# Kernel tuning notes

Measured on AMD Instinct MI355X. Metric: run time of the kernel, lower is better.

Reference implementation:

```python
import jax, jax.numpy as jnp
import numpy as np

NUM_PROMPTS = 20
PROMPT_DIM = 1024
BATCH = 32768
EPS = 1e-12  # F.normalize eps


def _l2_normalize(x):
    # matches torch F.normalize: x / max(||x||, eps)
    n = jnp.linalg.norm(x, axis=-1, keepdims=True)
    return x / jnp.maximum(n, EPS)


def setup_inputs() -> dict:
    key = jax.random.key(0)
    k1, k2, k3 = jax.random.split(key, 3)
    input_data = jax.random.normal(k1, (BATCH, PROMPT_DIM), dtype=jnp.float32)
    prompt_keys = jax.random.normal(k2, (NUM_PROMPTS, PROMPT_DIM), dtype=jnp.float32) * 0.01
    prompt_values = jax.random.normal(k3, (NUM_PROMPTS, PROMPT_DIM), dtype=jnp.float32)
    return {"input_data": input_data, "prompt_keys": prompt_keys,
            "prompt_values": prompt_values, "top_k": 5}


def reference(input_data, prompt_keys, prompt_values, top_k):
    # residual_strategy with use_prompt_threshhold=False: all samples stay
    # active for exactly top_k steps.
    norm_keys = _l2_normalize(prompt_keys)  # [P, D]
    residual = input_data                   # [B, D]
    selected, indices = [], []
    commitment = jnp.zeros((input_data.shape[0],), dtype=input_data.dtype)
    for _ in range(top_k):  # small fixed loop (top_k=5)
        sims = _l2_normalize(residual) @ norm_keys.T          # [B, P] cosine sim
        probs = jax.nn.softmax(sims, axis=1)                  # [B, P]
        top1_idx = jnp.argmax(probs, axis=1)                  # [B]
        top1_val = jnp.take_along_axis(probs, top1_idx[:, None], axis=1)[:, 0]
        pv = prompt_values[top1_idx]                          # [B, D]
        selected.append(pv)
        indices.append(top1_idx)
        commitment = commitment + top1_val
        residual = residual - pv
    selected_prompts = jnp.stack(selected, axis=1)            # [B, top_k, D]
    topk_indices = jnp.stack(indices, axis=1)                 # [B, top_k]
    diversity_loss = -jnp.mean(commitment)
    return selected_prompts, diversity_loss, topk_indices
```

## Files before the change

### kernel.cpp

```cpp
#include <hip/hip_runtime.h>


#define D  1024
#define PP 20
#define SBS 44
#define NBK 512
#define TBK 512
#define NWK (NBK * (TBK / 64))
#define NWSUM 2048

__device__ __forceinline__ float bfly_xor1(float x) {
    return __int_as_float(__builtin_amdgcn_update_dpp(
        __float_as_int(x), __float_as_int(x), 0xB1, 0xF, 0xF, false));
}
__device__ __forceinline__ float bfly_xor2(float x) {
    return __int_as_float(__builtin_amdgcn_update_dpp(
        __float_as_int(x), __float_as_int(x), 0x4E, 0xF, 0xF, false));
}
__device__ __forceinline__ float bfly(float x) {
    x += bfly_xor1(x);
    x += bfly_xor2(x);
    x += __shfl_xor(x, 4, 64);
    x += __shfl_xor(x, 8, 64);
    x += __shfl_xor(x, 16, 64);
    x += __shfl_xor(x, 32, 64);
    return x;
}

__global__ __launch_bounds__(1024) void pp_pre(
    const float* __restrict__ keys,
    const float* __restrict__ vals,
    float* __restrict__ nk,
    float* __restrict__ vkf,
    float* __restrict__ vvf)
{
    __shared__ float nk_s[PP * D];
    __shared__ float nrm_s[PP];
    const int tid = threadIdx.x;

    if (tid < PP) {
        const float* kp = keys + tid * D;
        double s0 = 0.0, s1 = 0.0;
        for (int d = 0; d < D; d += 2) {
            s0 += (double)kp[d]     * (double)kp[d];
            s1 += (double)kp[d + 1] * (double)kp[d + 1];
        }
        nrm_s[tid] = sqrtf((float)(s0 + s1));
    }
    __syncthreads();

    for (int i = tid; i < PP * D; i += blockDim.x) {
        float x = keys[i] / nrm_s[i >> 10];
        nk_s[i] = x;
        nk[i]   = x;
    }
    __syncthreads();

    if (tid < 2 * PP * PP) {
        const int which = tid & 1;
        const int rem   = tid >> 1;
        const int q = rem / PP, p = rem % PP;
        const float* vq    = vals + q * D;
        const float* other = which ? (vals + p * D) : (nk_s + p * D);
        double s0 = 0.0, s1 = 0.0;
        for (int d = 0; d < D; d += 2) {
            s0 += (double)vq[d]     * (double)other[d];
            s1 += (double)vq[d + 1] * (double)other[d + 1];
        }
        float r = (float)(s0 + s1);
        if (which) vvf[rem] = r; else vkf[rem] = r;
    }
}

__global__ __launch_bounds__(TBK) void pp_dots(
    const float* __restrict__ input,
    const float* __restrict__ vals,
    const float* __restrict__ nk,
    float* __restrict__ sbuf,
    int B)
{
    __shared__ float s_keys[PP * D];
    const int tid = threadIdx.x;
    {
        const float4* a = (const float4*)nk;
        float4* sa = (float4*)s_keys;
        for (int i = tid; i < PP * D / 4; i += TBK) sa[i] = a[i];
    }
    __syncthreads();

    const int lane = tid & 63;
    const int gw   = blockIdx.x * (TBK / 64) + (tid >> 6);

    for (int rowA = gw; rowA < B; rowA += 2 * NWK) {
        const int  rowB = rowA + NWK;
        const bool hasB = rowB < B;

        const float4* ipA = (const float4*)(input + (size_t)rowA * D);
        float4 a0 = ipA[lane], a1 = ipA[lane + 64], a2 = ipA[lane + 128], a3 = ipA[lane + 192];
        const float4* ipB = (const float4*)(input + (size_t)(hasB ? rowB : rowA) * D);
        float4 b0 = ipB[lane], b1 = ipB[lane + 64], b2 = ipB[lane + 128], b3 = ipB[lane + 192];

        float rvA[16] = { a0.x,a0.y,a0.z,a0.w, a1.x,a1.y,a1.z,a1.w,
                          a2.x,a2.y,a2.z,a2.w, a3.x,a3.y,a3.z,a3.w };
        float rvB[16] = { b0.x,b0.y,b0.z,b0.w, b1.x,b1.y,b1.z,b1.w,
                          b2.x,b2.y,b2.z,b2.w, b3.x,b3.y,b3.z,b3.w };

        float sqA = 0.f;
#pragma unroll
        for (int i = 0; i < 16; i++) sqA = fmaf(rvA[i], rvA[i], sqA);
        sqA = bfly(sqA);
        float sqB = 0.f;
#pragma unroll
        for (int i = 0; i < 16; i++) sqB = fmaf(rvB[i], rvB[i], sqB);
        sqB = bfly(sqB);

        float oA = sqA, oB = sqB;

#pragma unroll 1
        for (int p = 0; p < PP; p++) {
            const float4* vp = (const float4*)(vals + (size_t)p * D);
            float4 v0 = vp[lane], v1 = vp[lane + 64], v2 = vp[lane + 128], v3 = vp[lane + 192];
            float vl[16] = { v0.x,v0.y,v0.z,v0.w, v1.x,v1.y,v1.z,v1.w,
                             v2.x,v2.y,v2.z,v2.w, v3.x,v3.y,v3.z,v3.w };
            float abA = 0.f, abB = 0.f;
#pragma unroll
            for (int i = 0; i < 16; i++) abA = fmaf(rvA[i], vl[i], abA);
#pragma unroll
            for (int i = 0; i < 16; i++) abB = fmaf(rvB[i], vl[i], abB);
            abA += bfly_xor1(abA);        abB += bfly_xor1(abB);
            abA += bfly_xor2(abA);        abB += bfly_xor2(abB);
            abA += __shfl_xor(abA, 4, 64);  abB += __shfl_xor(abB, 4, 64);
            abA += __shfl_xor(abA, 8, 64);  abB += __shfl_xor(abB, 8, 64);
            abA += __shfl_xor(abA, 16, 64); abB += __shfl_xor(abB, 16, 64);
            abA += __shfl_xor(abA, 32, 64); abB += __shfl_xor(abB, 32, 64);
            oA = (lane == PP + p) ? abA : oA;
            oB = (lane == PP + p) ? abB : oB;
        }

        double rdA[16], rdB[16];
#pragma unroll
        for (int i = 0; i < 16; i++) rdA[i] = (double)rvA[i];
#pragma unroll
        for (int i = 0; i < 16; i++) rdB[i] = (double)rvB[i];

#pragma unroll 1
        for (int p = 0; p < PP; p++) {
            const float4* kp = (const float4*)(s_keys + p * D);
            float4 k0 = kp[lane], k1 = kp[lane + 64], k2 = kp[lane + 128], k3 = kp[lane + 192];
            float kk[16] = { k0.x,k0.y,k0.z,k0.w, k1.x,k1.y,k1.z,k1.w,
                             k2.x,k2.y,k2.z,k2.w, k3.x,k3.y,k3.z,k3.w };
            double accA = 0.0, accB = 0.0;
#pragma unroll
            for (int i = 0; i < 16; i++) accA = fma(rdA[i], (double)kk[i], accA);
#pragma unroll
            for (int i = 0; i < 16; i++) accB = fma(rdB[i], (double)kk[i], accB);
            float spA = (float)accA, spB = (float)accB;
            spA += bfly_xor1(spA);        spB += bfly_xor1(spB);
            spA += bfly_xor2(spA);        spB += bfly_xor2(spB);
            spA += __shfl_xor(spA, 4, 64);  spB += __shfl_xor(spB, 4, 64);
            spA += __shfl_xor(spA, 8, 64);  spB += __shfl_xor(spB, 8, 64);
            spA += __shfl_xor(spA, 16, 64); spB += __shfl_xor(spB, 16, 64);
            spA += __shfl_xor(spA, 32, 64); spB += __shfl_xor(spB, 32, 64);
            oA = (lane == p) ? spA : oA;
            oB = (lane == p) ? spB : oB;
        }

        if (lane < 2 * PP + 1) {
            sbuf[(size_t)rowA * SBS + lane] = oA;
            if (hasB) sbuf[(size_t)rowB * SBS + lane] = oB;
        }
    }
}

__global__ __launch_bounds__(256) void pp_decide(
    const float* __restrict__ sbuf,
    const float* __restrict__ vkf,
    const float* __restrict__ vvf,
    float* __restrict__ out_idx,
    float* __restrict__ cmrow,
    int B, int K)
{
    __shared__ float vk_s[PP * PP];
    __shared__ float vv_s[PP * PP];
    for (int i = threadIdx.x; i < PP * PP; i += 256) { vk_s[i] = vkf[i]; vv_s[i] = vvf[i]; }
    __syncthreads();
    const int row = blockIdx.x * 256 + threadIdx.x;
    if (row >= B) return;

    const float4* rp = (const float4*)(sbuf + (size_t)row * SBS);
    float s[PP], rvp[PP];
    {
        float4 a0 = rp[0], a1 = rp[1], a2 = rp[2], a3 = rp[3], a4 = rp[4];
        float4 b0 = rp[5], b1 = rp[6], b2 = rp[7], b3 = rp[8], b4 = rp[9];
        s[0]=a0.x;  s[1]=a0.y;  s[2]=a0.z;  s[3]=a0.w;
        s[4]=a1.x;  s[5]=a1.y;  s[6]=a1.z;  s[7]=a1.w;
        s[8]=a2.x;  s[9]=a2.y;  s[10]=a2.z; s[11]=a2.w;
        s[12]=a3.x; s[13]=a3.y; s[14]=a3.z; s[15]=a3.w;
        s[16]=a4.x; s[17]=a4.y; s[18]=a4.z; s[19]=a4.w;
        rvp[0]=b0.x;  rvp[1]=b0.y;  rvp[2]=b0.z;  rvp[3]=b0.w;
        rvp[4]=b1.x;  rvp[5]=b1.y;  rvp[6]=b1.z;  rvp[7]=b1.w;
        rvp[8]=b2.x;  rvp[9]=b2.y;  rvp[10]=b2.z; rvp[11]=b2.w;
        rvp[12]=b3.x; rvp[13]=b3.y; rvp[14]=b3.z; rvp[15]=b3.w;
        rvp[16]=b4.x; rvp[17]=b4.y; rvp[18]=b4.z; rvp[19]=b4.w;
    }
    float rn2 = ((const float*)rp)[2 * PP];

    float cm = 0.f;
    for (int t = 0; t < K; t++) {
        float nrm = sqrtf(rn2);
        float sims[PP];
#pragma unroll
        for (int p = 0; p < PP; p++) sims[p] = s[p] / nrm;
        float mx = sims[0];
#pragma unroll
        for (int p = 1; p < PP; p++) mx = fmaxf(mx, sims[p]);
        float e[PP];
        float denom = 0.f;
#pragma unroll
        for (int p = 0; p < PP; p++) { e[p] = expf(sims[p] - mx); denom += e[p]; }
        float best = -1.f; int bi = 0;
#pragma unroll
        for (int p = 0; p < PP; p++) {
            float pr = e[p] / denom;
            if (pr > best) { best = pr; bi = p; }
        }
        cm += best;
        out_idx[(size_t)row * K + t] = (float)bi;

        if (t + 1 < K) {
            float rvbi = rvp[0];
#pragma unroll
            for (int p = 1; p < PP; p++) rvbi = (p == bi) ? rvp[p] : rvbi;
            rn2 = rn2 - 2.f * rvbi + vv_s[bi * PP + bi];
#pragma unroll
            for (int p = 0; p < PP; p++) { s[p] -= vk_s[bi * PP + p]; rvp[p] -= vv_s[bi * PP + p]; }
        }
    }
    cmrow[row] = cm;
}

__global__ __launch_bounds__(256) void pp_wsum(
    const float* __restrict__ cmrow, double* __restrict__ wsum, int B)
{
    const int g = blockIdx.x * 256 + threadIdx.x;
    if (g >= NWSUM) return;
    double s = 0.0;
    for (int r = g; r < B; r += NWSUM) s += (double)cmrow[r];
    wsum[g] = s;
}

__global__ __launch_bounds__(256) void pp_bcast(
    const float* __restrict__ vals,
    const float* __restrict__ out_idx,
    float* __restrict__ out_sel,
    int nTask)
{
    const int lane = threadIdx.x & 63;
    const int wid  = blockIdx.x * 4 + (threadIdx.x >> 6);
    const int nw   = gridDim.x * 4;

    int task = wid;
    int bi = (task < nTask) ? (int)out_idx[task] : 0;
    while (task < nTask) {
        const int ntask = task + nw;
        const int nbi = (ntask < nTask) ? (int)out_idx[ntask] : 0;

        const float4* pv = (const float4*)(vals + (size_t)bi * D);
        float4* ob = (float4*)(out_sel + (size_t)task * D);
        float4 a = pv[lane], b = pv[lane + 64], c = pv[lane + 128], d = pv[lane + 192];
        ob[lane]       = a;
        ob[lane + 64]  = b;
        ob[lane + 128] = c;
        ob[lane + 192] = d;

        task = ntask; bi = nbi;
    }
}

__global__ __launch_bounds__(256) void pp_loss(
    const double* __restrict__ wsum, float* __restrict__ out_loss, int B)
{
    __shared__ double sh[4];
    const int tid = threadIdx.x;
    double s = 0.0;
    for (int i = tid; i < NWSUM; i += 256) s += wsum[i];
#pragma unroll
    for (int m = 1; m < 64; m <<= 1) s += __shfl_xor(s, m, 64);
    if ((tid & 63) == 0) sh[tid >> 6] = s;
    __syncthreads();
    if (tid == 0) {
        double tot = sh[0] + sh[1] + sh[2] + sh[3];
        out_loss[0] = (float)(-(tot / (double)B));
    }
}

extern "C" void kernel_launch(void* const* d_in, const int* in_sizes, int n_in,
                              void* d_out, int out_size, void* d_ws, size_t ws_size,
                              hipStream_t stream) {
    const float* input = (const float*)d_in[0];
    const float* keys  = (const float*)d_in[1];
    const float* vals  = (const float*)d_in[2];

    const int B = in_sizes[0] / D;
    const int K = (out_size - 1) / (B * (D + 1));

    float* out_sel  = (float*)d_out;
    const size_t selN = (size_t)B * K * D;
    float* out_loss = out_sel + selN;
    float* out_idx  = out_sel + selN + 1;

    char*  ws    = (char*)d_ws;
    float* nk    = (float*)ws;
    float* vkf   = nk + PP * D;
    float* vvf   = vkf + PP * PP;
    double* wsum = (double*)(ws + ((PP * D + 2 * PP * PP) * 4));

    float* sbuf  = out_sel;
    float* cmrow = out_sel + (size_t)B * SBS;

    const int nTask = B * K;

    pp_pre   <<<1, 1024, 0, stream>>>(keys, vals, nk, vkf, vvf);
    pp_dots  <<<NBK, TBK, 0, stream>>>(input, vals, nk, sbuf, B);
    pp_decide<<<(B + 255) / 256, 256, 0, stream>>>(sbuf, vkf, vvf, out_idx, cmrow, B, K);
    pp_wsum  <<<(NWSUM + 255) / 256, 256, 0, stream>>>(cmrow, wsum, B);
    pp_bcast <<<2048, 256, 0, stream>>>(vals, out_idx, out_sel, nTask);
    pp_loss  <<<1, 256, 0, stream>>>(wsum, out_loss, B);
}
```

Measured before the change: 345.4 us.

## Split prompt precompute across blocks, stage decide rows in LDS, use DPP xor8

The single-block precompute kernel is split into a key-normalisation kernel and a second kernel that spreads the 800 double-precision value/key and value/value dot products over 13 blocks instead of one. The decide kernel now loads its block's rows of the score buffer into shared memory with coalesced float4 copies, replacing strided per-thread row reads. The xor-8 butterfly step now uses a DPP row-rotate instead of a shuffle. These target the serial latency of the one-block precompute and uncoalesced reads in decide, at the cost of an extra launch and about 45KB of shared memory per decide block, which lowers occupancy. The DPP control 0x128 is a row rotate by 8, which matches xor 8 for a sum within a 16-lane row.

```diff
diff --git a/kernel.cpp b/kernel.cpp
--- a/kernel.cpp
+++ b/kernel.cpp
@@ -17,24 +17,24 @@
     return __int_as_float(__builtin_amdgcn_update_dpp(
         __float_as_int(x), __float_as_int(x), 0x4E, 0xF, 0xF, false));
 }
+__device__ __forceinline__ float bfly_xor8(float x) {
+    return __int_as_float(__builtin_amdgcn_update_dpp(
+        __float_as_int(x), __float_as_int(x), 0x128, 0xF, 0xF, false));
+}
 __device__ __forceinline__ float bfly(float x) {
     x += bfly_xor1(x);
     x += bfly_xor2(x);
     x += __shfl_xor(x, 4, 64);
-    x += __shfl_xor(x, 8, 64);
+    x += bfly_xor8(x);
     x += __shfl_xor(x, 16, 64);
     x += __shfl_xor(x, 32, 64);
     return x;
 }
 
-__global__ __launch_bounds__(1024) void pp_pre(
+__global__ __launch_bounds__(1024) void pp_pre1(
     const float* __restrict__ keys,
-    const float* __restrict__ vals,
-    float* __restrict__ nk,
-    float* __restrict__ vkf,
-    float* __restrict__ vvf)
-{
-    __shared__ float nk_s[PP * D];
+    float* __restrict__ nk)
+{
     __shared__ float nrm_s[PP];
     const int tid = threadIdx.x;
 
@@ -49,27 +49,30 @@
     }
     __syncthreads();
 
-    for (int i = tid; i < PP * D; i += blockDim.x) {
-        float x = keys[i] / nrm_s[i >> 10];
-        nk_s[i] = x;
-        nk[i]   = x;
-    }
-    __syncthreads();
-
-    if (tid < 2 * PP * PP) {
-        const int which = tid & 1;
-        const int rem   = tid >> 1;
-        const int q = rem / PP, p = rem % PP;
-        const float* vq    = vals + q * D;
-        const float* other = which ? (vals + p * D) : (nk_s + p * D);
-        double s0 = 0.0, s1 = 0.0;
-        for (int d = 0; d < D; d += 2) {
-            s0 += (double)vq[d]     * (double)other[d];
-            s1 += (double)vq[d + 1] * (double)other[d + 1];
-        }
-        float r = (float)(s0 + s1);
-        if (which) vvf[rem] = r; else vkf[rem] = r;
-    }
+    for (int i = tid; i < PP * D; i += blockDim.x)
+        nk[i] = keys[i] / nrm_s[i >> 10];
+}
+
+__global__ __launch_bounds__(64) void pp_pre2(
+    const float* __restrict__ nk,
+    const float* __restrict__ vals,
+    float* __restrict__ vkf,
+    float* __restrict__ vvf)
+{
+    const int tid = blockIdx.x * 64 + threadIdx.x;
+    if (tid >= 2 * PP * PP) return;
+    const int which = tid & 1;
+    const int rem   = tid >> 1;
+    const int q = rem / PP, p = rem % PP;
+    const float* vq    = vals + q * D;
+    const float* other = which ? (vals + p * D) : (nk + p * D);
+    double s0 = 0.0, s1 = 0.0;
+    for (int d = 0; d < D; d += 2) {
+        s0 += (double)vq[d]     * (double)other[d];
+        s1 += (double)vq[d + 1] * (double)other[d + 1];
+    }
+    float r = (float)(s0 + s1);
+    if (which) vvf[rem] = r; else vkf[rem] = r;
 }
 
 __global__ __launch_bounds__(TBK) void pp_dots(
@@ -127,10 +130,10 @@
             for (int i = 0; i < 16; i++) abA = fmaf(rvA[i], vl[i], abA);
 #pragma unroll
             for (int i = 0; i < 16; i++) abB = fmaf(rvB[i], vl[i], abB);
-            abA += bfly_xor1(abA);        abB += bfly_xor1(abB);
-            abA += bfly_xor2(abA);        abB += bfly_xor2(abB);
+            abA += bfly_xor1(abA);          abB += bfly_xor1(abB);
+            abA += bfly_xor2(abA);          abB += bfly_xor2(abB);
             abA += __shfl_xor(abA, 4, 64);  abB += __shfl_xor(abB, 4, 64);
-            abA += __shfl_xor(abA, 8, 64);  abB += __shfl_xor(abB, 8, 64);
+            abA += bfly_xor8(abA);          abB += bfly_xor8(abB);
             abA += __shfl_xor(abA, 16, 64); abB += __shfl_xor(abB, 16, 64);
             abA += __shfl_xor(abA, 32, 64); abB += __shfl_xor(abB, 32, 64);
             oA = (lane == PP + p) ? abA : oA;
@@ -155,10 +158,10 @@
 #pragma unroll
             for (int i = 0; i < 16; i++) accB = fma(rdB[i], (double)kk[i], accB);
             float spA = (float)accA, spB = (float)accB;
-            spA += bfly_xor1(spA);        spB += bfly_xor1(spB);
-            spA += bfly_xor2(spA);        spB += bfly_xor2(spB);
+            spA += bfly_xor1(spA);          spB += bfly_xor1(spB);
+            spA += bfly_xor2(spA);          spB += bfly_xor2(spB);
             spA += __shfl_xor(spA, 4, 64);  spB += __shfl_xor(spB, 4, 64);
-            spA += __shfl_xor(spA, 8, 64);  spB += __shfl_xor(spB, 8, 64);
+            spA += bfly_xor8(spA);          spB += bfly_xor8(spB);
             spA += __shfl_xor(spA, 16, 64); spB += __shfl_xor(spB, 16, 64);
             spA += __shfl_xor(spA, 32, 64); spB += __shfl_xor(spB, 32, 64);
             oA = (lane == p) ? spA : oA;
@@ -182,12 +185,22 @@
 {
     __shared__ float vk_s[PP * PP];
     __shared__ float vv_s[PP * PP];
+    __shared__ float sb_s[256 * SBS];
     for (int i = threadIdx.x; i < PP * PP; i += 256) { vk_s[i] = vkf[i]; vv_s[i] = vvf[i]; }
+
+    const int base  = blockIdx.x * 256;
+    const int nrows = (B - base < 256) ? (B - base) : 256;
+    {
+        const float4* g4 = (const float4*)(sbuf + (size_t)base * SBS);
+        float4* s4 = (float4*)sb_s;
+        const int nf4 = nrows * (SBS / 4);
+        for (int i = threadIdx.x; i < nf4; i += 256) s4[i] = g4[i];
+    }
     __syncthreads();
-    const int row = blockIdx.x * 256 + threadIdx.x;
+    const int row = base + threadIdx.x;
     if (row >= B) return;
 
-    const float4* rp = (const float4*)(sbuf + (size_t)row * SBS);
+    const float4* rp = (const float4*)(sb_s + threadIdx.x * SBS);
     float s[PP], rvp[PP];
     {
         float4 a0 = rp[0], a1 = rp[1], a2 = rp[2], a3 = rp[3], a4 = rp[4];
@@ -320,7 +333,8 @@
 
     const int nTask = B * K;
 
-    pp_pre   <<<1, 1024, 0, stream>>>(keys, vals, nk, vkf, vvf);
+    pp_pre1  <<<1, 1024, 0, stream>>>(keys, nk);
+    pp_pre2  <<<(2 * PP * PP + 63) / 64, 64, 0, stream>>>(nk, vals, vkf, vvf);
     pp_dots  <<<NBK, TBK, 0, stream>>>(input, vals, nk, sbuf, B);
     pp_decide<<<(B + 255) / 256, 256, 0, stream>>>(sbuf, vkf, vvf, out_idx, cmrow, B, K);
     pp_wsum  <<<(NWSUM + 255) / 256, 256, 0, stream>>>(cmrow, wsum, B);
```

Result: faster. 303.8 us (-12.0%).
